# Optimization experiments

Measured on AMD Instinct MI355X. Metric: run time of the kernel, lower is better.

The kernel has to match this reference:

```python
import jax, jax.numpy as jnp
import numpy as np

OUT_SIZE = 7
SPATIAL_SCALE = 0.0625
SAMPLE_NUM = 2


def setup_inputs() -> dict:
    key = jax.random.key(0)
    k1, k2, k3, k4, k5, k6 = jax.random.split(key, 6)
    N, C, H, W = 4, 256, 96, 96
    K = 1024
    features = jax.random.normal(k1, (N, C, H, W), dtype=jnp.float32)
    img_h, img_w = H / SPATIAL_SCALE, W / SPATIAL_SCALE
    batch_idx = jax.random.randint(k2, (K,), 0, N).astype(jnp.float32)
    x1 = jax.random.uniform(k3, (K,)) * (img_w - 320.0)
    y1 = jax.random.uniform(k4, (K,)) * (img_h - 320.0)
    x2 = x1 + 16.0 + jax.random.uniform(k5, (K,)) * 300.0
    y2 = y1 + 16.0 + jax.random.uniform(k6, (K,)) * 300.0
    rois = jnp.stack([batch_idx, x1, y1, x2, y2], axis=1).astype(jnp.float32)
    return {"features": features, "rois": rois}


def _sample_coords(start, bin_size):
    # start, bin_size: [K]; returns [K, OUT_SIZE*SAMPLE_NUM] sample-point coords
    g = jnp.arange(OUT_SIZE * SAMPLE_NUM, dtype=jnp.float32)
    bin_idx = jnp.floor(g / SAMPLE_NUM)
    sub = g - bin_idx * SAMPLE_NUM
    offs = bin_idx + (sub + 0.5) / SAMPLE_NUM
    return start[:, None] + bin_size[:, None] * offs[None, :]


def _interp_1d(coord, size):
    # coord: [K, G] sample coords along one axis of a map of length `size`.
    valid = (coord >= -1.0) & (coord <= jnp.float32(size))
    c = jnp.clip(coord, 0.0, jnp.float32(size - 1))
    lo = jnp.floor(c)
    hi = jnp.minimum(lo + 1.0, jnp.float32(size - 1))
    frac = c - lo  # weight of hi; (1-frac) weight of lo
    return lo.astype(jnp.int32), hi.astype(jnp.int32), frac, valid


def roi_align(features, rois):
    N, C, H, W = features.shape
    b = rois[:, 0].astype(jnp.int32)
    x1, y1, x2, y2 = (rois[:, i] * SPATIAL_SCALE for i in (1, 2, 3, 4))
    roi_w = jnp.maximum(x2 - x1, 1.0)
    roi_h = jnp.maximum(y2 - y1, 1.0)
    bin_w = roi_w / OUT_SIZE
    bin_h = roi_h / OUT_SIZE

    ys = _sample_coords(y1, bin_h)  # [K, G]
    xs = _sample_coords(x1, bin_w)  # [K, G]
    ylo, yhi, fy, vy = _interp_1d(ys, H)
    xlo, xhi, fx, vx = _interp_1d(xs, W)

    bb = b[:, None, None]

    def gather(yi, xi):
        # -> [K, G, G, C]
        return features[bb, :, yi[:, :, None], xi[:, None, :]]

    wy_lo, wy_hi = (1.0 - fy), fy
    wx_lo, wx_hi = (1.0 - fx), fx

    def w2(wy, wx):
        return (wy[:, :, None] * wx[:, None, :])[..., None]

    val = (gather(ylo, xlo) * w2(wy_lo, wx_lo)
           + gather(ylo, xhi) * w2(wy_lo, wx_hi)
           + gather(yhi, xlo) * w2(wy_hi, wx_lo)
           + gather(yhi, xhi) * w2(wy_hi, wx_hi))
    mask = (vy[:, :, None] & vx[:, None, :])[..., None]
    val = jnp.where(mask, val, 0.0)

    K = rois.shape[0]
    G = OUT_SIZE * SAMPLE_NUM
    val = val.reshape(K, OUT_SIZE, SAMPLE_NUM, OUT_SIZE, SAMPLE_NUM, C)
    out = val.mean(axis=(2, 4))          # average the sample points per bin
    return jnp.transpose(out, (0, 3, 1, 2))  # [K, C, out, out]


def reference(features, rois):
    return roi_align(features, rois)
```

## Files before the change

### kernel.cpp

```cpp
#include <hip/hip_runtime.h>

#define CCH   256
#define FH    96
#define FW    96
#define HW    (FH*FW)
#define SCALE 0.0625f

#define HROWS 21
#define SQMAX 7
#define PLANE (HROWS*SQMAX*4)
#define WCH   32

__global__ __launch_bounds__(256, 8)
void roialign_kernel(const float* __restrict__ feat,
                     const float* __restrict__ rois,
                     float* __restrict__ out)
{
    __shared__ __align__(16) float win[4 * PLANE];
    __shared__ int   s_lo[2][14];
    __shared__ float s_wl[2][14], s_wh[2][14];

    const int k    = blockIdx.x >> 1;
    const int half = blockIdx.x & 1;
    const int tid  = threadIdx.x;
    const int w    = tid >> 6;
    const int ll   = tid & 63;

    const float x1 = rois[k*5+1] * SCALE;
    const float y1 = rois[k*5+2] * SCALE;
    const float x2 = rois[k*5+3] * SCALE;
    const float y2 = rois[k*5+4] * SCALE;
    const int   b  = (int)rois[k*5+0];
    const float binw = fmaxf(x2 - x1, 1.0f) * (1.0f/7.0f);
    const float binh = fmaxf(y2 - y1, 1.0f) * (1.0f/7.0f);

    if (tid < 28) {
        const int   axis  = (tid >= 14) ? 1 : 0;
        const int   g     = axis ? tid - 14 : tid;
        const float start = axis ? x1 : y1;
        const float bsz   = axis ? binw : binh;
        const float offs  = (float)(g >> 1) + 0.25f + 0.5f*(float)(g & 1);
        const float coord = start + bsz * offs;
        const bool  valid = (coord >= -1.0f) && (coord <= 96.0f);
        const float cc    = fminf(fmaxf(coord, 0.0f), 95.0f);
        const float lof   = floorf(cc);
        const float frac  = cc - lof;
        const float v     = valid ? 1.0f : 0.0f;
        s_lo[axis][g] = (int)lof;
        s_wl[axis][g] = (1.0f - frac) * v;
        s_wh[axis][g] = frac * v;
    }
    __syncthreads();

    const int row0   = s_lo[0][0];
    const int col0   = s_lo[1][0] & ~3;
    const int colEnd = min(s_lo[1][13] + 1, FW-1);
    const int width  = colEnd - col0 + 1;
    const int cwq    = min((width + 3) >> 2, 6);
    const int sQ     = ((cwq + 1) & ~1) | 1;
    const int RS     = sQ * 4;
    int hw_          = min(s_lo[0][13] + 1, FH-1) - row0 + 1;
    const int hwin   = min(hw_, HROWS);
    const int nslot  = hwin * cwq;

    float* const wp = &win[w * PLANE];

    {
        const float4 z = make_float4(0.f, 0.f, 0.f, 0.f);
        #pragma unroll
        for (int j = 0; j < 3; ++j) {
            const int q = ll + 64*j;
            if (q < PLANE/4) *(float4*)&wp[q*4] = z;
        }
    }

    const bool active = ll < 49;
    const int  p  = active ? ll : 0;
    const int  oy = p / 7;
    const int  ox = p - oy*7;

    int   aL[4], aH[4];
    float w00[4], w01[4], w10[4], w11[4];
    #pragma unroll
    for (int sy = 0; sy < 2; ++sy) {
        const int   gy  = 2*oy + sy;
        const int   rlo = min(s_lo[0][gy] - row0,                 HROWS-1);
        const int   rhi = min(min(s_lo[0][gy]+1, FH-1) - row0,    HROWS-1);
        const float wyl = s_wl[0][gy], wyh = s_wh[0][gy];
        #pragma unroll
        for (int sx = 0; sx < 2; ++sx) {
            const int   gx  = 2*ox + sx;
            const int   clo = min(s_lo[1][gx] - col0, RS-2);
            const float wxl = s_wl[1][gx], wxh = s_wh[1][gx];
            const int   s   = sy*2 + sx;
            aL[s] = rlo*RS + clo;
            aH[s] = rhi*RS + clo;
            w00[s] = wyl*wxl*0.25f;  w01[s] = wyl*wxh*0.25f;
            w10[s] = wyh*wxl*0.25f;  w11[s] = wyh*wxh*0.25f;
        }
    }

    const int  sl1 = ll + 64;
    const int  r0  = ll  / cwq, q0 = ll  - r0*cwq;
    const int  r1  = sl1 / cwq, q1 = sl1 - r1*cwq;
    const bool L0  = ll  < nslot;
    const bool L1  = sl1 < nslot;
    const int  goff0 = min(row0 + r0, FH-1)*FW + col0 + q0*4;
    const int  goff1 = min(row0 + r1, FH-1)*FW + col0 + q1*4;
    const int  ld0   = min(r0, HROWS-1)*RS + q0*4;
    const int  ld1   = min(r1, HROWS-1)*RS + q1*4;

    const int    cb   = half*128 + w*WCH;
    const float* gch  = feat + (size_t)(b*CCH + cb) * HW;
    float*       outp = out  + ((size_t)k*CCH + cb)*49 + p;

    float4 st0, st1;
    if (L0) st0 = *(const float4*)(gch + goff0);
    if (L1) st1 = *(const float4*)(gch + goff1);

    for (int c = 0; c < WCH; ++c) {
        if (L0) *(float4*)&wp[ld0] = st0;
        if (L1) *(float4*)&wp[ld1] = st1;

        if (c + 1 < WCH) {
            const float* gn = gch + (size_t)(c+1)*HW;
            if (L0) st0 = *(const float4*)(gn + goff0);
            if (L1) st1 = *(const float4*)(gn + goff1);
        }

        if (active) {
            float t0 = w00[0]*wp[aL[0]]   + w01[0]*wp[aL[0]+1]
                     + w10[0]*wp[aH[0]]   + w11[0]*wp[aH[0]+1];
            float t1 = w00[1]*wp[aL[1]]   + w01[1]*wp[aL[1]+1]
                     + w10[1]*wp[aH[1]]   + w11[1]*wp[aH[1]+1];
            float t2 = w00[2]*wp[aL[2]]   + w01[2]*wp[aL[2]+1]
                     + w10[2]*wp[aH[2]]   + w11[2]*wp[aH[2]+1];
            float t3 = w00[3]*wp[aL[3]]   + w01[3]*wp[aL[3]+1]
                     + w10[3]*wp[aH[3]]   + w11[3]*wp[aH[3]+1];
            outp[0] = (t0 + t1) + (t2 + t3);
        }
        outp += 49;
    }
}

extern "C" void kernel_launch(void* const* d_in, const int* in_sizes, int n_in,
                              void* d_out, int out_size, void* d_ws, size_t ws_size,
                              hipStream_t stream) {
    const float* feat = (const float*)d_in[0];
    const float* rois = (const float*)d_in[1];
    float*       outp = (float*)d_out;
    const int K = in_sizes[1] / 5;
    roialign_kernel<<<K*2, 256, 0, stream>>>(feat, rois, outp);
}
```

Measured before the change: 131.4 us.

## Bucket ROIs by batch image and map blocks to XCDs for L2 locality

Adds a small pre-pass kernel that groups ROI indices by batch image into a permutation in workspace. The main kernel then remaps block IDs so that, given round-robin block dispatch across the 8 XCDs, each XCD handles ROIs from one image and one channel half. The aim is to keep each XCD's L2 working set to a single feature map slice and cut redundant fetches from far memory. The cost is an extra kernel launch and an indirect load per block. The index mapping hardcodes 256 blocks per XCD pair, so it is only correct for K=1024.

After: 132.0 us. Within noise of the previous version (+0.4%).

```diff
diff --git a/kernel.cpp b/kernel.cpp
--- a/kernel.cpp
+++ b/kernel.cpp
@@ -11,17 +11,43 @@
 #define PLANE (HROWS*SQMAX*4)
 #define WCH   32
 
+__global__ void bucket_rois(const float* __restrict__ rois, int* __restrict__ perm, int K)
+{
+    __shared__ int cnt[4], base[4];
+    const int t = threadIdx.x;
+    if (t < 4) cnt[t] = 0;
+    __syncthreads();
+    int b = 0, pos = 0;
+    if (t < K) {
+        b   = min(max((int)rois[t*5], 0), 3);
+        pos = atomicAdd(&cnt[b], 1);
+    }
+    __syncthreads();
+    if (t == 0) {
+        int s = 0;
+        #pragma unroll
+        for (int i = 0; i < 4; ++i) { base[i] = s; s += cnt[i]; }
+    }
+    __syncthreads();
+    if (t < K) perm[base[b] + pos] = t;
+}
+
 __global__ __launch_bounds__(256, 8)
 void roialign_kernel(const float* __restrict__ feat,
                      const float* __restrict__ rois,
-                     float* __restrict__ out)
+                     float* __restrict__ out,
+                     const int* __restrict__ perm)
 {
     __shared__ __align__(16) float win[4 * PLANE];
     __shared__ int   s_lo[2][14];
     __shared__ float s_wl[2][14], s_wh[2][14];
 
-    const int k    = blockIdx.x >> 1;
-    const int half = blockIdx.x & 1;
+    const int xcd  = blockIdx.x & 7;
+    const int j    = blockIdx.x >> 3;
+    const int q    = ((xcd >> 1) << 8) + j;
+    const int half = xcd & 1;
+    const int k    = perm ? perm[q] : q;
+
     const int tid  = threadIdx.x;
     const int w    = tid >> 6;
     const int ll   = tid & 63;
@@ -68,9 +94,9 @@
     {
         const float4 z = make_float4(0.f, 0.f, 0.f, 0.f);
         #pragma unroll
-        for (int j = 0; j < 3; ++j) {
-            const int q = ll + 64*j;
-            if (q < PLANE/4) *(float4*)&wp[q*4] = z;
+        for (int jj = 0; jj < 3; ++jj) {
+            const int qq = ll + 64*jj;
+            if (qq < PLANE/4) *(float4*)&wp[qq*4] = z;
         }
     }
 
@@ -150,5 +176,11 @@
     const float* rois = (const float*)d_in[1];
     float*       outp = (float*)d_out;
     const int K = in_sizes[1] / 5;
-    roialign_kernel<<<K*2, 256, 0, stream>>>(feat, rois, outp);
+
+    int* perm = nullptr;
+    if (d_ws && ws_size >= (size_t)K * sizeof(int) && K <= 1024) {
+        perm = (int*)d_ws;
+        bucket_rois<<<1, 1024, 0, stream>>>(rois, perm, K);
+    }
+    roialign_kernel<<<K*2, 256, 0, stream>>>(feat, rois, outp, perm);
 }
```

## Stage ROI windows via async global-to-LDS loads with triple-buffered pipeline

Applied to the files above, without the earlier changes.

Replaces the register-staged global loads and LDS stores with __builtin_amdgcn_global_load_lds direct copies into a three-plane ring buffer per wave. Hand-placed s_waitcnt vmcnt counts let loads for up to two channels ahead overlap with interpolation of the current channel. The window zeroing is dropped and slot indices are clamped instead. LDS use per block grows and occupancy bounds drop from 8 to 6. The code relies on exact vmcnt counting, which also has to account for the output stores, and on in-wave ordering of the LDS writes without a barrier.

Result: slower. 134.2 us (+2.1%).

```diff
diff --git a/kernel.cpp b/kernel.cpp
--- a/kernel.cpp
+++ b/kernel.cpp
@@ -7,16 +7,26 @@
 #define SCALE 0.0625f
 
 #define HROWS 21
-#define SQMAX 7
-#define PLANE (HROWS*SQMAX*4)
+#define PSLOT 128
+#define NPLN  3
+#define WVF   (NPLN*PSLOT*4)
 #define WCH   32
 
-__global__ __launch_bounds__(256, 8)
+#define GLOBAL_AS __attribute__((address_space(1)))
+#define LDS_AS    __attribute__((address_space(3)))
+
+__device__ __forceinline__ void async16(const float* g, float* l) {
+    __builtin_amdgcn_global_load_lds((const GLOBAL_AS void*)g, (LDS_AS void*)l, 16, 0, 0);
+}
+
+#define VMW(n) asm volatile("s_waitcnt vmcnt(" #n ")" ::: "memory")
+
+__global__ __launch_bounds__(256, 6)
 void roialign_kernel(const float* __restrict__ feat,
                      const float* __restrict__ rois,
                      float* __restrict__ out)
 {
-    __shared__ __align__(16) float win[4 * PLANE];
+    __shared__ __align__(16) float win[4 * WVF];
     __shared__ int   s_lo[2][14];
     __shared__ float s_wl[2][14], s_wh[2][14];
 
@@ -57,22 +67,15 @@
     const int colEnd = min(s_lo[1][13] + 1, FW-1);
     const int width  = colEnd - col0 + 1;
     const int cwq    = min((width + 3) >> 2, 6);
-    const int sQ     = ((cwq + 1) & ~1) | 1;
-    const int RS     = sQ * 4;
+    int sQ           = ((cwq + 1) & ~1) | 1;
     int hw_          = min(s_lo[0][13] + 1, FH-1) - row0 + 1;
     const int hwin   = min(hw_, HROWS);
-    const int nslot  = hwin * cwq;
+    if (hwin * sQ > PSLOT) sQ = cwq;
+    const int RS     = sQ * 4;
+    const int nslotS = hwin * sQ;
+    const bool LI2   = (nslotS > 64);
 
-    float* const wp = &win[w * PLANE];
-
-    {
-        const float4 z = make_float4(0.f, 0.f, 0.f, 0.f);
-        #pragma unroll
-        for (int j = 0; j < 3; ++j) {
-            const int q = ll + 64*j;
-            if (q < PLANE/4) *(float4*)&wp[q*4] = z;
-        }
-    }
+    float* const wp = &win[w * WVF];
 
     const bool active = ll < 49;
     const int  p  = active ? ll : 0;
@@ -84,8 +87,8 @@
     #pragma unroll
     for (int sy = 0; sy < 2; ++sy) {
         const int   gy  = 2*oy + sy;
-        const int   rlo = min(s_lo[0][gy] - row0,                 HROWS-1);
-        const int   rhi = min(min(s_lo[0][gy]+1, FH-1) - row0,    HROWS-1);
+        const int   rlo = min(s_lo[0][gy] - row0,              hwin-1);
+        const int   rhi = min(min(s_lo[0][gy]+1, FH-1) - row0, hwin-1);
         const float wyl = s_wl[0][gy], wyh = s_wh[0][gy];
         #pragma unroll
         for (int sx = 0; sx < 2; ++sx) {
@@ -100,47 +103,64 @@
         }
     }
 
-    const int  sl1 = ll + 64;
-    const int  r0  = ll  / cwq, q0 = ll  - r0*cwq;
-    const int  r1  = sl1 / cwq, q1 = sl1 - r1*cwq;
-    const bool L0  = ll  < nslot;
-    const bool L1  = sl1 < nslot;
-    const int  goff0 = min(row0 + r0, FH-1)*FW + col0 + q0*4;
-    const int  goff1 = min(row0 + r1, FH-1)*FW + col0 + q1*4;
-    const int  ld0   = min(r0, HROWS-1)*RS + q0*4;
-    const int  ld1   = min(r1, HROWS-1)*RS + q1*4;
+    int soff0, soff1;
+    {
+        const int s0 = ll,      r0 = s0 / sQ, q0 = s0 - r0*sQ;
+        const int s1 = ll + 64, r1 = s1 / sQ, q1 = s1 - r1*sQ;
+        const int rc0 = min(r0, hwin-1), qc0 = min(q0, cwq-1);
+        const int rc1 = min(r1, hwin-1), qc1 = min(q1, cwq-1);
+        soff0 = min(row0 + rc0, FH-1)*FW + col0 + qc0*4;
+        soff1 = min(row0 + rc1, FH-1)*FW + col0 + qc1*4;
+    }
 
     const int    cb   = half*128 + w*WCH;
     const float* gch  = feat + (size_t)(b*CCH + cb) * HW;
     float*       outp = out  + ((size_t)k*CCH + cb)*49 + p;
 
-    float4 st0, st1;
-    if (L0) st0 = *(const float4*)(gch + goff0);
-    if (L1) st1 = *(const float4*)(gch + goff1);
+#define STAGE(cc, pl) do {                                              \
+        const float* gs_ = gch + (size_t)(cc) * HW;                     \
+        float* lp_ = wp + (pl) * (PSLOT*4);                             \
+        async16(gs_ + soff0, lp_);                                      \
+        if (LI2) async16(gs_ + soff1, lp_ + 256);                       \
+    } while (0)
 
-    for (int c = 0; c < WCH; ++c) {
-        if (L0) *(float4*)&wp[ld0] = st0;
-        if (L1) *(float4*)&wp[ld1] = st1;
+#define COMP(pl) do {                                                   \
+        const float* bp_ = wp + (pl) * (PSLOT*4);                       \
+        if (active) {                                                   \
+            float t0 = w00[0]*bp_[aL[0]] + w01[0]*bp_[aL[0]+1]          \
+                     + w10[0]*bp_[aH[0]] + w11[0]*bp_[aH[0]+1];         \
+            float t1 = w00[1]*bp_[aL[1]] + w01[1]*bp_[aL[1]+1]          \
+                     + w10[1]*bp_[aH[1]] + w11[1]*bp_[aH[1]+1];         \
+            float t2 = w00[2]*bp_[aL[2]] + w01[2]*bp_[aL[2]+1]          \
+                     + w10[2]*bp_[aH[2]] + w11[2]*bp_[aH[2]+1];         \
+            float t3 = w00[3]*bp_[aL[3]] + w01[3]*bp_[aL[3]+1]          \
+                     + w10[3]*bp_[aH[3]] + w11[3]*bp_[aH[3]+1];         \
+            outp[0] = (t0 + t1) + (t2 + t3);                            \
+        }                                                               \
+        outp += 49;                                                     \
+    } while (0)
 
-        if (c + 1 < WCH) {
-            const float* gn = gch + (size_t)(c+1)*HW;
-            if (L0) st0 = *(const float4*)(gn + goff0);
-            if (L1) st1 = *(const float4*)(gn + goff1);
-        }
+#define PIPE(N0, N1, NS, NT) do {                                       \
+        STAGE(0, 0); STAGE(1, 1);                                       \
+        STAGE(2, 2); VMW(N0); COMP(0);                                  \
+        STAGE(3, 0); VMW(N1); COMP(1);                                  \
+        int pl = 2, sp = 0;                                             \
+        for (int c = 2; c < WCH-2; ++c) {                               \
+            sp = (sp == 2) ? 0 : sp + 1;                                \
+            STAGE(c+2, sp);                                             \
+            VMW(NS); COMP(pl);                                          \
+            pl = (pl == 2) ? 0 : pl + 1;                                \
+        }                                                               \
+        VMW(NT); COMP(pl); pl = (pl == 2) ? 0 : pl + 1;                 \
+        VMW(2);  COMP(pl);                                              \
+    } while (0)
 
-        if (active) {
-            float t0 = w00[0]*wp[aL[0]]   + w01[0]*wp[aL[0]+1]
-                     + w10[0]*wp[aH[0]]   + w11[0]*wp[aH[0]+1];
-            float t1 = w00[1]*wp[aL[1]]   + w01[1]*wp[aL[1]+1]
-                     + w10[1]*wp[aH[1]]   + w11[1]*wp[aH[1]+1];
-            float t2 = w00[2]*wp[aL[2]]   + w01[2]*wp[aL[2]+1]
-                     + w10[2]*wp[aH[2]]   + w11[2]*wp[aH[2]+1];
-            float t3 = w00[3]*wp[aL[3]]   + w01[3]*wp[aL[3]+1]
-                     + w10[3]*wp[aH[3]]   + w11[3]*wp[aH[3]+1];
-            outp[0] = (t0 + t1) + (t2 + t3);
-        }
-        outp += 49;
-    }
+    if (!LI2) PIPE(2, 3, 4, 3);
+    else      PIPE(4, 5, 6, 4);
+
+#undef STAGE
+#undef COMP
+#undef PIPE
 }
 
 extern "C" void kernel_launch(void* const* d_in, const int* in_sizes, int n_in,
```
